# Kernel tuning notes

Measured on AMD Instinct MI355X. Metric: run time of the kernel, lower is better.

The kernel has to match this reference:

```python
import jax, jax.numpy as jnp
import numpy as np

B, S, H, E = 2, 4096, 2048, 8


def setup_inputs() -> dict:
    key = jax.random.key(0)
    k1, k2, k3 = jax.random.split(key, 3)
    x = jax.random.normal(k1, (B, S, H), dtype=jnp.float32)
    w_router = jax.random.normal(k2, (E, H), dtype=jnp.float32) * (1.0 / np.sqrt(H))
    # nn.Linear weight layout: [out_features, in_features] per expert -> [E, H, H]
    w_experts = jax.random.normal(k3, (E, H, H), dtype=jnp.float32) * (1.0 / np.sqrt(H))
    return {"x": x, "w_router": w_router, "w_experts": w_experts}


def reference(x, w_router, w_experts):
    # router logits: x @ W_r^T  -> [B, S, E]
    logits = jnp.einsum('bsh,eh->bse', x, w_router)
    idx = jnp.argmax(logits, axis=-1)  # [B, S] top-1 expert per token
    # dense all-expert outputs (matches original which evaluates every expert):
    # expert_e(x) = x @ W_e^T -> [B, S, E, H]
    all_out = jnp.einsum('bsh,efh->bsef', x, w_experts)
    # masked sum over one-hot mask == gather of the selected expert output
    out = jnp.take_along_axis(all_out, idx[:, :, None, None], axis=2)[:, :, 0, :]
    return out
```

## Files before the change

### kernel.cpp

```cpp
#include <hip/hip_runtime.h>
#include <hip/hip_bf16.h>
#include <cstdint>

#define T_TOK 8192
#define H_DIM 2048
#define N_EXP 8
#define FLAGBIT 0x80000000u

typedef __attribute__((ext_vector_type(4))) float f32x4;
typedef __attribute__((ext_vector_type(8))) short bf16x8;

__device__ __forceinline__ unsigned short f2bf(float f) {
  unsigned int u = __builtin_bit_cast(unsigned int, f);
  u += 0x7fffu + ((u >> 16) & 1u);
  return (unsigned short)(u >> 16);
}

#define GLL(SRC, DST) __builtin_amdgcn_global_load_lds( \
    (const __attribute__((address_space(1))) void*)(SRC), \
    (__attribute__((address_space(3))) void*)(DST), 16, 0, 0)

__global__ __launch_bounds__(256, 2) void k_conv(const float* __restrict__ we,
                                                 unsigned short* __restrict__ wb) {
  const size_t tix = ((size_t)blockIdx.x * 256 + threadIdx.x) * 8;
  const size_t stride = (size_t)2048 * 256 * 8;
  f32x4 v[16];
#pragma unroll
  for (int it = 0; it < 8; ++it) {
    v[2 * it]     = *reinterpret_cast<const f32x4*>(we + tix + (size_t)it * stride);
    v[2 * it + 1] = *reinterpret_cast<const f32x4*>(we + tix + (size_t)it * stride + 4);
  }
#pragma unroll
  for (int q = 0; q < 16; ++q) asm volatile("" : "+v"(v[q]));
#pragma unroll
  for (int it = 0; it < 8; ++it) {
    union { unsigned short h[8]; uint4 u; } r;
#pragma unroll
    for (int q = 0; q < 4; ++q) {
      r.h[q]     = f2bf(v[2 * it][q]);
      r.h[4 + q] = f2bf(v[2 * it + 1][q]);
    }
    *reinterpret_cast<uint4*>(wb + tix + (size_t)it * stride) = r.u;
  }
}

__global__ __launch_bounds__(256) void k_router(const float* __restrict__ x,
    const float* __restrict__ wr, unsigned short* __restrict__ xb,
    int* __restrict__ idx)
{
  __shared__ float swr[N_EXP * H_DIM];
#pragma unroll
  for (int i = 0; i < 16; ++i) {
    const int o = (threadIdx.x + i * 256) * 4;
    *reinterpret_cast<float4*>(&swr[o]) = *reinterpret_cast<const float4*>(&wr[o]);
  }
  __syncthreads();
  const int wv = threadIdx.x >> 6, lane = threadIdx.x & 63;
  const int t0 = (blockIdx.x * 4 + wv) * 4;
  float acc[4][N_EXP];
#pragma unroll
  for (int tt = 0; tt < 4; ++tt)
#pragma unroll
    for (int e = 0; e < N_EXP; ++e) acc[tt][e] = 0.f;
#pragma unroll
  for (int c = 0; c < H_DIM / 256; ++c) {
    const int h = c * 256 + lane * 4;
    float4 wvv[N_EXP];
#pragma unroll
    for (int e = 0; e < N_EXP; ++e)
      wvv[e] = *reinterpret_cast<const float4*>(&swr[e * H_DIM + h]);
#pragma unroll
    for (int tt = 0; tt < 4; ++tt) {
      const float4 xv = *reinterpret_cast<const float4*>(x + (size_t)(t0 + tt) * H_DIM + h);
      ushort4 bv;
      bv.x = f2bf(xv.x); bv.y = f2bf(xv.y); bv.z = f2bf(xv.z); bv.w = f2bf(xv.w);
      *reinterpret_cast<ushort4*>(xb + (size_t)(t0 + tt) * H_DIM + h) = bv;
#pragma unroll
      for (int e = 0; e < N_EXP; ++e) {
        acc[tt][e] = fmaf(xv.x, wvv[e].x, acc[tt][e]);
        acc[tt][e] = fmaf(xv.y, wvv[e].y, acc[tt][e]);
        acc[tt][e] = fmaf(xv.z, wvv[e].z, acc[tt][e]);
        acc[tt][e] = fmaf(xv.w, wvv[e].w, acc[tt][e]);
      }
    }
  }
#pragma unroll
  for (int off = 32; off >= 1; off >>= 1)
#pragma unroll
    for (int tt = 0; tt < 4; ++tt)
#pragma unroll
      for (int e = 0; e < N_EXP; ++e) acc[tt][e] += __shfl_xor(acc[tt][e], off, 64);
  if (lane == 0) {
#pragma unroll
    for (int tt = 0; tt < 4; ++tt) {
      float best = acc[tt][0]; int be = 0;
#pragma unroll
      for (int e = 1; e < N_EXP; ++e) if (acc[tt][e] > best) { best = acc[tt][e]; be = e; }
      idx[t0 + tt] = be;
    }
  }
}

__global__ __launch_bounds__(1024) void k_sort(const int* __restrict__ idx,
    int* __restrict__ tlist, int* __restrict__ estar, int* __restrict__ mlo,
    int* __restrict__ mhi, int* __restrict__ rpos, int* __restrict__ rtile,
    int* __restrict__ rtc)
{
  __shared__ int wc[N_EXP][128];
  __shared__ int wbase[N_EXP][128];
  __shared__ int sTot[N_EXP];
  __shared__ int off[N_EXP + 1];
  __shared__ int sE[32], sCnt[N_EXP], sBase[N_EXP];
  const int tid = threadIdx.x, w = tid >> 6, l = tid & 63;
  int myE[8];
#pragma unroll
  for (int j = 0; j < 8; ++j) {
    myE[j] = idx[j * 1024 + tid];
#pragma unroll
    for (int e = 0; e < N_EXP; ++e) {
      const unsigned long long bm = __ballot(myE[j] == e);
      if (l == e) wc[e][j * 16 + w] = __popcll(bm);
    }
  }
  __syncthreads();
  if (tid < N_EXP) {
    int s = 0;
    for (int k = 0; k < 128; ++k) { wbase[tid][k] = s; s += wc[tid][k]; }
    sTot[tid] = s;
  }
  __syncthreads();
  if (tid == 0) {
    off[0] = 0;
    for (int e = 0; e < N_EXP; ++e) off[e + 1] = off[e] + sTot[e];
  }
  __syncthreads();
#pragma unroll
  for (int j = 0; j < 8; ++j) {
    int rank = 0;
#pragma unroll
    for (int e = 0; e < N_EXP; ++e) {
      const unsigned long long bm = __ballot(myE[j] == e);
      if (myE[j] == e) rank = __popcll(bm & ((1ull << l) - 1ull));
    }
    tlist[off[myE[j]] + wbase[myE[j]][j * 16 + w] + rank] = j * 1024 + tid;
  }
  if (tid < 32) {
    const int lo = tid * 256, hi = lo + 256;
    int bl = -1, bE = 0, bLo = 0, bHi = 0;
#pragma unroll
    for (int e = 0; e < N_EXP; ++e) {
      const int a = off[e] > lo ? off[e] : lo;
      const int b = off[e + 1] < hi ? off[e + 1] : hi;
      if (b - a > bl) { bl = b - a; bE = e; bLo = a - lo; bHi = b - lo; }
    }
    sE[tid] = bE; estar[tid] = bE; mlo[tid] = bLo; mhi[tid] = bHi;
  }
  __syncthreads();
  if (tid < N_EXP) {
    int cnt = 0;
    for (int t = 0; t < 32; ++t) {
      if (sE[t] == tid) continue;
      const int lo = t * 256, hi = lo + 256;
      const int a = off[tid] > lo ? off[tid] : lo;
      const int b = off[tid + 1] < hi ? off[tid + 1] : hi;
      if (b > a) cnt += b - a;
    }
    sCnt[tid] = cnt;
  }
  __syncthreads();
  if (tid == 0) {
    int base = 0, ntile = 0;
    for (int e = 0; e < N_EXP; ++e) {
      sBase[e] = base;
      const int pt = (sCnt[e] + 127) >> 7;
      for (int k = 0; k < pt; ++k) rtile[ntile++] = e;
      base += pt << 7;
    }
    *rtc = ntile;
  }
  __syncthreads();
  if (tid < N_EXP && sCnt[tid] > 0) {
    int ptr = sBase[tid], firstp = -1;
    for (int t = 0; t < 32; ++t) {
      if (sE[t] == tid) continue;
      const int lo = t * 256, hi = lo + 256;
      const int a = off[tid] > lo ? off[tid] : lo;
      const int b = off[tid + 1] < hi ? off[tid + 1] : hi;
      for (int p = a; p < b; ++p) { if (firstp < 0) firstp = p; rpos[ptr++] = p; }
    }
    const int end = sBase[tid] + (((sCnt[tid] + 127) >> 7) << 7);
    for (; ptr < end; ++ptr) rpos[ptr] = (int)((unsigned)firstp | FLAGBIT);
  }
}

__global__ __launch_bounds__(256) void k_zero_min(const int* __restrict__ rpos,
    const int* __restrict__ tlist, const int* __restrict__ rtc,
    float* __restrict__ out)
{
  const int nslots = (*rtc) << 7;
  const float4 z = {0.f, 0.f, 0.f, 0.f};
  for (int s = blockIdx.x; s < nslots; s += 256) {
    const int ent = rpos[s];
    if ((unsigned)ent & FLAGBIT) continue;
    const int tok = tlist[ent];
    float* op = out + (size_t)tok * H_DIM;
    for (int i = threadIdx.x; i < H_DIM / 4; i += 256)
      reinterpret_cast<float4*>(op)[i] = z;
  }
}

template<int Q, bool LOADB, bool VMC>
__device__ __forceinline__ void gphase(const char* LP,
    __attribute__((address_space(3))) char* LDS3,
    int rdBase, int aRowOff, int bRowOff, int ch0, int ch1,
    bf16x8 (&bfr)[8], f32x4 (&acc)[8][4],
    const unsigned short* s0, const unsigned short* s1, int d0, int d1)
{
  if constexpr (LOADB) {
#pragma unroll
    for (int nf = 0; nf < 4; ++nf) {
      bfr[nf * 2 + 0] = *reinterpret_cast<const bf16x8*>(LP + rdBase + 32768 + bRowOff + nf * 2048 + ch0);
      bfr[nf * 2 + 1] = *reinterpret_cast<const bf16x8*>(LP + rdBase + 32768 + bRowOff + nf * 2048 + ch1);
    }
  }
  bf16x8 af[2][2];
#pragma unroll
  for (int m = 0; m < 2; ++m) {
    af[m][0] = *reinterpret_cast<const bf16x8*>(LP + rdBase + aRowOff + (2 * Q + m) * 2048 + ch0);
    af[m][1] = *reinterpret_cast<const bf16x8*>(LP + rdBase + aRowOff + (2 * Q + m) * 2048 + ch1);
  }
  GLL(s0, LDS3 + d0);
  GLL(s1, LDS3 + d1);
  __builtin_amdgcn_sched_barrier(0);
  __builtin_amdgcn_s_barrier();
  __builtin_amdgcn_sched_barrier(0);
  __builtin_amdgcn_s_setprio(1);
#pragma unroll
  for (int ks = 0; ks < 2; ++ks)
#pragma unroll
    for (int m = 0; m < 2; ++m)
#pragma unroll
      for (int nf = 0; nf < 4; ++nf)
        acc[2 * Q + m][nf] = __builtin_amdgcn_mfma_f32_16x16x32_bf16(af[m][ks], bfr[nf * 2 + ks], acc[2 * Q + m][nf], 0, 0, 0);
  __builtin_amdgcn_s_setprio(0);
  if constexpr (VMC) asm volatile("s_waitcnt vmcnt(4)" ::: "memory");
  __builtin_amdgcn_sched_barrier(0);
  __builtin_amdgcn_s_barrier();
  __builtin_amdgcn_sched_barrier(0);
}

__global__ __launch_bounds__(512, 2) void k_gemm(const unsigned short* __restrict__ xb,
    const unsigned short* __restrict__ wb, const int* __restrict__ tlist,
    const int* __restrict__ estar, const int* __restrict__ mlo, const int* __restrict__ mhi,
    const int* __restrict__ rpos, const int* __restrict__ rtile, const int* __restrict__ rtc,
    float* __restrict__ out)
{
  __shared__ short lds[65536];
  const int bid = blockIdx.x;
  const int tid = threadIdx.x;
  const int l = tid & 63, wv = tid >> 6;
  const int l16 = l & 15, g = l >> 4;
  const char* LP = (const char*)lds;
  auto* LDS3 = (__attribute__((address_space(3))) char*)lds;
  const int sw = l16 & 7;
  const int ch0 = ((0 + g) ^ sw) << 4;
  const int ch1 = ((4 + g) ^ sw) << 4;
  const int csrc = ((l & 7) ^ ((l >> 3) & 7)) * 8;
  const int srow = l >> 3;

  if (bid < 256) {
    const int mt = (bid & 7) * 4 + ((bid >> 3) & 3);
    const int nt = bid >> 5;
    const int m0 = mt * 256, f0 = nt * 256;
    const int e = estar[mt], mLo = mlo[mt], mHi = mhi[mt];
    const int wm = wv >> 2, wn = wv & 3;
    const int aRowOff = (wm * 128 + l16) * 128;
    const int bRowOff = (wn * 64 + l16) * 128;

    const unsigned short* aP[2][2];
    const unsigned short* bP[2][2];
    const unsigned short* wpan = wb + (size_t)e * H_DIM * H_DIM;
#pragma unroll
    for (int h = 0; h < 2; ++h)
#pragma unroll
      for (int j = 0; j < 2; ++j) {
        const int tok = tlist[m0 + h * 128 + (wv * 2 + j) * 8 + srow];
        aP[h][j] = xb + (size_t)tok * H_DIM + csrc;
        bP[h][j] = wpan + (size_t)(f0 + h * 128 + (wv * 2 + j) * 8 + srow) * H_DIM + csrc;
      }
    const int sl0 = wv * 2048, sl1 = wv * 2048 + 1024;

    f32x4 acc[8][4];
#pragma unroll
    for (int mf = 0; mf < 8; ++mf)
#pragma unroll
      for (int nf = 0; nf < 4; ++nf) acc[mf][nf] = (f32x4){0.f, 0.f, 0.f, 0.f};
    bf16x8 bfr[8];

    GLL(aP[0][0], LDS3 + 0 + sl0);      GLL(aP[0][1], LDS3 + 0 + sl1);
    GLL(aP[1][0], LDS3 + 16384 + sl0);  GLL(aP[1][1], LDS3 + 16384 + sl1);
    GLL(bP[0][0], LDS3 + 32768 + sl0);  GLL(bP[0][1], LDS3 + 32768 + sl1);
    GLL(bP[1][0], LDS3 + 49152 + sl0);  GLL(bP[1][1], LDS3 + 49152 + sl1);
    GLL(bP[0][0] + 64, LDS3 + 65536 + 32768 + sl0);  GLL(bP[0][1] + 64, LDS3 + 65536 + 32768 + sl1);
    GLL(bP[1][0] + 64, LDS3 + 65536 + 49152 + sl0);  GLL(bP[1][1] + 64, LDS3 + 65536 + 49152 + sl1);
    asm volatile("s_waitcnt vmcnt(4)" ::: "memory");
    __builtin_amdgcn_sched_barrier(0);
    __builtin_amdgcn_s_barrier();
    __builtin_amdgcn_sched_barrier(0);

    for (int i = 0; i < 16; ++i) {
      const int kk1 = ((2 * i + 1) << 6) & (H_DIM - 1);
      const int kk2 = ((2 * i + 2) << 6) & (H_DIM - 1);
      const int kk3 = ((2 * i + 3) << 6) & (H_DIM - 1);
      gphase<0, true , false>(LP, LDS3, 0, aRowOff, bRowOff, ch0, ch1, bfr, acc,
          aP[0][0] + kk1, aP[0][1] + kk1, 65536 + 0 + sl0, 65536 + 0 + sl1);
      gphase<1, false, false>(LP, LDS3, 0, aRowOff, bRowOff, ch0, ch1, bfr, acc,
          aP[1][0] + kk1, aP[1][1] + kk1, 65536 + 16384 + sl0, 65536 + 16384 + sl1);
      gphase<2, false, false>(LP, LDS3, 0, aRowOff, bRowOff, ch0, ch1, bfr, acc,
          bP[0][0] + kk2, bP[0][1] + kk2, 0 + 32768 + sl0, 0 + 32768 + sl1);
      gphase<3, false, true >(LP, LDS3, 0, aRowOff, bRowOff, ch0, ch1, bfr, acc,
          bP[1][0] + kk2, bP[1][1] + kk2, 0 + 49152 + sl0, 0 + 49152 + sl1);
      gphase<0, true , false>(LP, LDS3, 65536, aRowOff, bRowOff, ch0, ch1, bfr, acc,
          aP[0][0] + kk2, aP[0][1] + kk2, 0 + 0 + sl0, 0 + 0 + sl1);
      gphase<1, false, false>(LP, LDS3, 65536, aRowOff, bRowOff, ch0, ch1, bfr, acc,
          aP[1][0] + kk2, aP[1][1] + kk2, 0 + 16384 + sl0, 0 + 16384 + sl1);
      gphase<2, false, false>(LP, LDS3, 65536, aRowOff, bRowOff, ch0, ch1, bfr, acc,
          bP[0][0] + kk3, bP[0][1] + kk3, 65536 + 32768 + sl0, 65536 + 32768 + sl1);
      gphase<3, false, true >(LP, LDS3, 65536, aRowOff, bRowOff, ch0, ch1, bfr, acc,
          bP[1][0] + kk3, bP[1][1] + kk3, 65536 + 49152 + sl0, 65536 + 49152 + sl1);
    }

#pragma unroll
    for (int mf = 0; mf < 8; ++mf) {
#pragma unroll
      for (int r = 0; r < 4; ++r) {
        const int row = wm * 128 + mf * 16 + g * 4 + r;
        if (row >= mLo && row < mHi) {
          const int t = tlist[m0 + row];
          float* op = out + (size_t)t * H_DIM + f0 + wn * 64 + l16;
#pragma unroll
          for (int nf = 0; nf < 4; ++nf) op[nf * 16] = acc[mf][nf][r];
        }
      }
    }
    return;
  }

  const int bid2 = bid - 256;
  const int bx = bid2 >> 4;
  if (bx >= *rtc) return;
  const int f0 = ((bid2 >> 1) & 7) * 256;
  const int kc = bid2 & 1;
  const int e = rtile[bx];
  const int wm = wv >> 2, wn = wv & 3;

  const unsigned short* aS[2];
#pragma unroll
  for (int j = 0; j < 2; ++j) {
    const int ent = rpos[bx * 128 + (wv * 2 + j) * 8 + srow];
    const int tok = tlist[ent & 0x7fffffff];
    aS[j] = xb + (size_t)tok * H_DIM + csrc;
  }
  const unsigned short* bS[4];
#pragma unroll
  for (int j = 0; j < 4; ++j)
    bS[j] = wb + (size_t)e * H_DIM * H_DIM + (size_t)(f0 + (wv * 4 + j) * 8 + srow) * H_DIM + csrc;

  f32x4 acc[4][4];
#pragma unroll
  for (int mf = 0; mf < 4; ++mf)
#pragma unroll
    for (int nf = 0; nf < 4; ++nf) acc[mf][nf] = (f32x4){0.f, 0.f, 0.f, 0.f};

  for (int it = 0; it < 16; ++it) {
    const int kk = kc * 1024 + it * 64;
    __syncthreads();
#pragma unroll
    for (int j = 0; j < 2; ++j) GLL(aS[j] + kk, LDS3 + (wv * 2 + j) * 1024);
#pragma unroll
    for (int j = 0; j < 4; ++j) GLL(bS[j] + kk, LDS3 + 16384 + (wv * 4 + j) * 1024);
    __syncthreads();
    bf16x8 af[4][2];
#pragma unroll
    for (int mf = 0; mf < 4; ++mf) {
      af[mf][0] = *reinterpret_cast<const bf16x8*>(LP + (wm * 64 + mf * 16 + l16) * 128 + ch0);
      af[mf][1] = *reinterpret_cast<const bf16x8*>(LP + (wm * 64 + mf * 16 + l16) * 128 + ch1);
    }
#pragma unroll
    for (int nf = 0; nf < 4; ++nf) {
      const bf16x8 b0 = *reinterpret_cast<const bf16x8*>(LP + 16384 + (wn * 64 + nf * 16 + l16) * 128 + ch0);
      const bf16x8 b1 = *reinterpret_cast<const bf16x8*>(LP + 16384 + (wn * 64 + nf * 16 + l16) * 128 + ch1);
#pragma unroll
      for (int mf = 0; mf < 4; ++mf) {
        acc[mf][nf] = __builtin_amdgcn_mfma_f32_16x16x32_bf16(af[mf][0], b0, acc[mf][nf], 0, 0, 0);
        acc[mf][nf] = __builtin_amdgcn_mfma_f32_16x16x32_bf16(af[mf][1], b1, acc[mf][nf], 0, 0, 0);
      }
    }
  }
#pragma unroll
  for (int mf = 0; mf < 4; ++mf) {
#pragma unroll
    for (int r = 0; r < 4; ++r) {
      const int row = wm * 64 + mf * 16 + g * 4 + r;
      const int ent = rpos[bx * 128 + row];
      if (!((unsigned)ent & FLAGBIT)) {
        const int tok = tlist[ent];
        float* op = out + (size_t)tok * H_DIM + f0 + wn * 64 + l16;
#pragma unroll
        for (int nf = 0; nf < 4; ++nf) atomicAdd(op + nf * 16, acc[mf][nf][r]);
      }
    }
  }
}

extern "C" void kernel_launch(void* const* d_in, const int* in_sizes, int n_in,
                              void* d_out, int out_size, void* d_ws, size_t ws_size,
                              hipStream_t stream) {
  const float* x  = (const float*)d_in[0];
  const float* wr = (const float*)d_in[1];
  const float* we = (const float*)d_in[2];
  float* out = (float*)d_out;

  char* p = (char*)d_ws;
  unsigned short* xb = (unsigned short*)p; p += (size_t)T_TOK * H_DIM * 2;
  unsigned short* wb = (unsigned short*)p; p += (size_t)N_EXP * H_DIM * H_DIM * 2;
  int* idx    = (int*)p; p += T_TOK * 4;
  int* tlist  = (int*)p; p += T_TOK * 4;
  int* rpos   = (int*)p; p += T_TOK * 4;
  int* estar  = (int*)p; p += 32 * 4;
  int* mlo    = (int*)p; p += 32 * 4;
  int* mhi    = (int*)p; p += 32 * 4;
  int* rtile  = (int*)p; p += 64 * 4;
  int* rtc    = (int*)p; p += 64;

  k_conv<<<2048, 256, 0, stream>>>(we, wb);
  k_router<<<512, 256, 0, stream>>>(x, wr, xb, idx);
  k_sort<<<1, 1024, 0, stream>>>(idx, tlist, estar, mlo, mhi, rpos, rtile, rtc);
  k_zero_min<<<256, 256, 0, stream>>>(rpos, tlist, rtc, out);
  k_gemm<<<256 + 1024, 512, 0, stream>>>(xb, wb, tlist, estar, mlo, mhi, rpos, rtile, rtc, out);
}
```

Baseline: 194.1 us.

## Retile expert GEMM to 16 waves with 4-stage K-ring buffer

```diff
diff --git a/kernel.cpp b/kernel.cpp
--- a/kernel.cpp
+++ b/kernel.cpp
@@ -209,47 +209,7 @@
   }
 }
 
-template<int Q, bool LOADB, bool VMC>
-__device__ __forceinline__ void gphase(const char* LP,
-    __attribute__((address_space(3))) char* LDS3,
-    int rdBase, int aRowOff, int bRowOff, int ch0, int ch1,
-    bf16x8 (&bfr)[8], f32x4 (&acc)[8][4],
-    const unsigned short* s0, const unsigned short* s1, int d0, int d1)
-{
-  if constexpr (LOADB) {
-#pragma unroll
-    for (int nf = 0; nf < 4; ++nf) {
-      bfr[nf * 2 + 0] = *reinterpret_cast<const bf16x8*>(LP + rdBase + 32768 + bRowOff + nf * 2048 + ch0);
-      bfr[nf * 2 + 1] = *reinterpret_cast<const bf16x8*>(LP + rdBase + 32768 + bRowOff + nf * 2048 + ch1);
-    }
-  }
-  bf16x8 af[2][2];
-#pragma unroll
-  for (int m = 0; m < 2; ++m) {
-    af[m][0] = *reinterpret_cast<const bf16x8*>(LP + rdBase + aRowOff + (2 * Q + m) * 2048 + ch0);
-    af[m][1] = *reinterpret_cast<const bf16x8*>(LP + rdBase + aRowOff + (2 * Q + m) * 2048 + ch1);
-  }
-  GLL(s0, LDS3 + d0);
-  GLL(s1, LDS3 + d1);
-  __builtin_amdgcn_sched_barrier(0);
-  __builtin_amdgcn_s_barrier();
-  __builtin_amdgcn_sched_barrier(0);
-  __builtin_amdgcn_s_setprio(1);
-#pragma unroll
-  for (int ks = 0; ks < 2; ++ks)
-#pragma unroll
-    for (int m = 0; m < 2; ++m)
-#pragma unroll
-      for (int nf = 0; nf < 4; ++nf)
-        acc[2 * Q + m][nf] = __builtin_amdgcn_mfma_f32_16x16x32_bf16(af[m][ks], bfr[nf * 2 + ks], acc[2 * Q + m][nf], 0, 0, 0);
-  __builtin_amdgcn_s_setprio(0);
-  if constexpr (VMC) asm volatile("s_waitcnt vmcnt(4)" ::: "memory");
-  __builtin_amdgcn_sched_barrier(0);
-  __builtin_amdgcn_s_barrier();
-  __builtin_amdgcn_sched_barrier(0);
-}
-
-__global__ __launch_bounds__(512, 2) void k_gemm(const unsigned short* __restrict__ xb,
+__global__ __launch_bounds__(1024, 4) void k_gemm(const unsigned short* __restrict__ xb,
     const unsigned short* __restrict__ wb, const int* __restrict__ tlist,
     const int* __restrict__ estar, const int* __restrict__ mlo, const int* __restrict__ mhi,
     const int* __restrict__ rpos, const int* __restrict__ rtile, const int* __restrict__ rtc,
@@ -259,14 +219,9 @@
   const int bid = blockIdx.x;
   const int tid = threadIdx.x;
   const int l = tid & 63, wv = tid >> 6;
-  const int l16 = l & 15, g = l >> 4;
+  const int l16 = l & 15, g16 = l >> 4;
   const char* LP = (const char*)lds;
   auto* LDS3 = (__attribute__((address_space(3))) char*)lds;
-  const int sw = l16 & 7;
-  const int ch0 = ((0 + g) ^ sw) << 4;
-  const int ch1 = ((4 + g) ^ sw) << 4;
-  const int csrc = ((l & 7) ^ ((l >> 3) & 7)) * 8;
-  const int srow = l >> 3;
 
   if (bid < 256) {
     const int mt = (bid & 7) * 4 + ((bid >> 3) & 3);
@@ -274,70 +229,71 @@
     const int m0 = mt * 256, f0 = nt * 256;
     const int e = estar[mt], mLo = mlo[mt], mHi = mhi[mt];
     const int wm = wv >> 2, wn = wv & 3;
-    const int aRowOff = (wm * 128 + l16) * 128;
-    const int bRowOff = (wn * 64 + l16) * 128;
-
-    const unsigned short* aP[2][2];
-    const unsigned short* bP[2][2];
-    const unsigned short* wpan = wb + (size_t)e * H_DIM * H_DIM;
-#pragma unroll
-    for (int h = 0; h < 2; ++h)
-#pragma unroll
-      for (int j = 0; j < 2; ++j) {
-        const int tok = tlist[m0 + h * 128 + (wv * 2 + j) * 8 + srow];
-        aP[h][j] = xb + (size_t)tok * H_DIM + csrc;
-        bP[h][j] = wpan + (size_t)(f0 + h * 128 + (wv * 2 + j) * 8 + srow) * H_DIM + csrc;
-      }
-    const int sl0 = wv * 2048, sl1 = wv * 2048 + 1024;
-
-    f32x4 acc[8][4];
-#pragma unroll
-    for (int mf = 0; mf < 8; ++mf)
+
+    const int ch = (g16 ^ ((l16 >> 1) & 3)) << 4;
+    const int aRd = (wm * 64 + l16) * 64 + ch;
+    const int bRd = 16384 + (wn * 64 + l16) * 64 + ch;
+
+    const int csrc = (((l & 3) ^ ((l >> 3) & 3))) * 8;
+    const int srow = l >> 2;
+    const int tokA = tlist[m0 + wv * 16 + srow];
+    const unsigned short* aS = xb + (size_t)tokA * H_DIM + csrc;
+    const unsigned short* bS = wb + (size_t)e * H_DIM * H_DIM
+                                  + (size_t)(f0 + wv * 16 + srow) * H_DIM + csrc;
+    const int dA = wv * 1024;
+    const int dB = 16384 + wv * 1024;
+
+    f32x4 acc[4][4];
+#pragma unroll
+    for (int mf = 0; mf < 4; ++mf)
 #pragma unroll
       for (int nf = 0; nf < 4; ++nf) acc[mf][nf] = (f32x4){0.f, 0.f, 0.f, 0.f};
-    bf16x8 bfr[8];
-
-    GLL(aP[0][0], LDS3 + 0 + sl0);      GLL(aP[0][1], LDS3 + 0 + sl1);
-    GLL(aP[1][0], LDS3 + 16384 + sl0);  GLL(aP[1][1], LDS3 + 16384 + sl1);
-    GLL(bP[0][0], LDS3 + 32768 + sl0);  GLL(bP[0][1], LDS3 + 32768 + sl1);
-    GLL(bP[1][0], LDS3 + 49152 + sl0);  GLL(bP[1][1], LDS3 + 49152 + sl1);
-    GLL(bP[0][0] + 64, LDS3 + 65536 + 32768 + sl0);  GLL(bP[0][1] + 64, LDS3 + 65536 + 32768 + sl1);
-    GLL(bP[1][0] + 64, LDS3 + 65536 + 49152 + sl0);  GLL(bP[1][1] + 64, LDS3 + 65536 + 49152 + sl1);
+
+    GLL(aS +  0, LDS3 + 0 * 32768 + dA);  GLL(bS +  0, LDS3 + 0 * 32768 + dB);
+    GLL(aS + 32, LDS3 + 1 * 32768 + dA);  GLL(bS + 32, LDS3 + 1 * 32768 + dB);
+    GLL(aS + 64, LDS3 + 2 * 32768 + dA);  GLL(bS + 64, LDS3 + 2 * 32768 + dB);
     asm volatile("s_waitcnt vmcnt(4)" ::: "memory");
     __builtin_amdgcn_sched_barrier(0);
     __builtin_amdgcn_s_barrier();
     __builtin_amdgcn_sched_barrier(0);
 
-    for (int i = 0; i < 16; ++i) {
-      const int kk1 = ((2 * i + 1) << 6) & (H_DIM - 1);
-      const int kk2 = ((2 * i + 2) << 6) & (H_DIM - 1);
-      const int kk3 = ((2 * i + 3) << 6) & (H_DIM - 1);
-      gphase<0, true , false>(LP, LDS3, 0, aRowOff, bRowOff, ch0, ch1, bfr, acc,
-          aP[0][0] + kk1, aP[0][1] + kk1, 65536 + 0 + sl0, 65536 + 0 + sl1);
-      gphase<1, false, false>(LP, LDS3, 0, aRowOff, bRowOff, ch0, ch1, bfr, acc,
-          aP[1][0] + kk1, aP[1][1] + kk1, 65536 + 16384 + sl0, 65536 + 16384 + sl1);
-      gphase<2, false, false>(LP, LDS3, 0, aRowOff, bRowOff, ch0, ch1, bfr, acc,
-          bP[0][0] + kk2, bP[0][1] + kk2, 0 + 32768 + sl0, 0 + 32768 + sl1);
-      gphase<3, false, true >(LP, LDS3, 0, aRowOff, bRowOff, ch0, ch1, bfr, acc,
-          bP[1][0] + kk2, bP[1][1] + kk2, 0 + 49152 + sl0, 0 + 49152 + sl1);
-      gphase<0, true , false>(LP, LDS3, 65536, aRowOff, bRowOff, ch0, ch1, bfr, acc,
-          aP[0][0] + kk2, aP[0][1] + kk2, 0 + 0 + sl0, 0 + 0 + sl1);
-      gphase<1, false, false>(LP, LDS3, 65536, aRowOff, bRowOff, ch0, ch1, bfr, acc,
-          aP[1][0] + kk2, aP[1][1] + kk2, 0 + 16384 + sl0, 0 + 16384 + sl1);
-      gphase<2, false, false>(LP, LDS3, 65536, aRowOff, bRowOff, ch0, ch1, bfr, acc,
-          bP[0][0] + kk3, bP[0][1] + kk3, 65536 + 32768 + sl0, 65536 + 32768 + sl1);
-      gphase<3, false, true >(LP, LDS3, 65536, aRowOff, bRowOff, ch0, ch1, bfr, acc,
-          bP[1][0] + kk3, bP[1][1] + kk3, 65536 + 49152 + sl0, 65536 + 49152 + sl1);
-    }
-
-#pragma unroll
-    for (int mf = 0; mf < 8; ++mf) {
+    for (int t = 0; t < 64; ++t) {
+      const int buf  = (t & 3) * 32768;
+      const int nbuf = ((t + 3) & 3) * 32768;
+      const int kk   = ((t + 3) & 63) * 32;
+      bf16x8 af[4], bf[4];
+#pragma unroll
+      for (int mf = 0; mf < 4; ++mf)
+        af[mf] = *reinterpret_cast<const bf16x8*>(LP + buf + aRd + mf * 1024);
+#pragma unroll
+      for (int nf = 0; nf < 4; ++nf)
+        bf[nf] = *reinterpret_cast<const bf16x8*>(LP + buf + bRd + nf * 1024);
+      GLL(aS + kk, LDS3 + nbuf + dA);
+      GLL(bS + kk, LDS3 + nbuf + dB);
+      __builtin_amdgcn_sched_barrier(0);
+      __builtin_amdgcn_s_barrier();
+      __builtin_amdgcn_sched_barrier(0);
+      __builtin_amdgcn_s_setprio(1);
+#pragma unroll
+      for (int mf = 0; mf < 4; ++mf)
+#pragma unroll
+        for (int nf = 0; nf < 4; ++nf)
+          acc[mf][nf] = __builtin_amdgcn_mfma_f32_16x16x32_bf16(af[mf], bf[nf], acc[mf][nf], 0, 0, 0);
+      __builtin_amdgcn_s_setprio(0);
+      asm volatile("s_waitcnt vmcnt(4)" ::: "memory");
+      __builtin_amdgcn_sched_barrier(0);
+      __builtin_amdgcn_s_barrier();
+      __builtin_amdgcn_sched_barrier(0);
+    }
+
+#pragma unroll
+    for (int mf = 0; mf < 4; ++mf) {
 #pragma unroll
       for (int r = 0; r < 4; ++r) {
-        const int row = wm * 128 + mf * 16 + g * 4 + r;
+        const int row = wm * 64 + mf * 16 + g16 * 4 + r;
         if (row >= mLo && row < mHi) {
-          const int t = tlist[m0 + row];
-          float* op = out + (size_t)t * H_DIM + f0 + wn * 64 + l16;
+          const int t2 = tlist[m0 + row];
+          float* op = out + (size_t)t2 * H_DIM + f0 + wn * 64 + l16;
 #pragma unroll
           for (int nf = 0; nf < 4; ++nf) op[nf * 16] = acc[mf][nf][r];
         }
@@ -353,55 +309,56 @@
   const int kc = bid2 & 1;
   const int e = rtile[bx];
   const int wm = wv >> 2, wn = wv & 3;
-
-  const unsigned short* aS[2];
-#pragma unroll
-  for (int j = 0; j < 2; ++j) {
-    const int ent = rpos[bx * 128 + (wv * 2 + j) * 8 + srow];
+  const int sw = l16 & 7;
+  const int ch0 = ((0 + g16) ^ sw) << 4, ch1 = ((4 + g16) ^ sw) << 4;
+  const int csrc8 = ((l & 7) ^ ((l >> 3) & 7)) * 8;
+  const int srow8 = l >> 3;
+
+  const unsigned short* aS;
+  {
+    const int ent = rpos[bx * 128 + wv * 8 + srow8];
     const int tok = tlist[ent & 0x7fffffff];
-    aS[j] = xb + (size_t)tok * H_DIM + csrc;
-  }
-  const unsigned short* bS[4];
-#pragma unroll
-  for (int j = 0; j < 4; ++j)
-    bS[j] = wb + (size_t)e * H_DIM * H_DIM + (size_t)(f0 + (wv * 4 + j) * 8 + srow) * H_DIM + csrc;
-
-  f32x4 acc[4][4];
-#pragma unroll
-  for (int mf = 0; mf < 4; ++mf)
+    aS = xb + (size_t)tok * H_DIM + csrc8;
+  }
+  const unsigned short* bS0 = wb + (size_t)e * H_DIM * H_DIM
+                                 + (size_t)(f0 + wv * 8 + srow8) * H_DIM + csrc8;
+  const unsigned short* bS1 = bS0 + (size_t)128 * H_DIM;
+
+  f32x4 acc[2][4];
+#pragma unroll
+  for (int mf = 0; mf < 2; ++mf)
 #pragma unroll
     for (int nf = 0; nf < 4; ++nf) acc[mf][nf] = (f32x4){0.f, 0.f, 0.f, 0.f};
 
   for (int it = 0; it < 16; ++it) {
     const int kk = kc * 1024 + it * 64;
     __syncthreads();
-#pragma unroll
-    for (int j = 0; j < 2; ++j) GLL(aS[j] + kk, LDS3 + (wv * 2 + j) * 1024);
-#pragma unroll
-    for (int j = 0; j < 4; ++j) GLL(bS[j] + kk, LDS3 + 16384 + (wv * 4 + j) * 1024);
+    GLL(aS + kk, LDS3 + wv * 1024);
+    GLL(bS0 + kk, LDS3 + 16384 + wv * 1024);
+    GLL(bS1 + kk, LDS3 + 16384 + 16384 + wv * 1024);
     __syncthreads();
-    bf16x8 af[4][2];
-#pragma unroll
-    for (int mf = 0; mf < 4; ++mf) {
-      af[mf][0] = *reinterpret_cast<const bf16x8*>(LP + (wm * 64 + mf * 16 + l16) * 128 + ch0);
-      af[mf][1] = *reinterpret_cast<const bf16x8*>(LP + (wm * 64 + mf * 16 + l16) * 128 + ch1);
+    bf16x8 af[2][2];
+#pragma unroll
+    for (int mf = 0; mf < 2; ++mf) {
+      af[mf][0] = *reinterpret_cast<const bf16x8*>(LP + (wm * 32 + mf * 16 + l16) * 128 + ch0);
+      af[mf][1] = *reinterpret_cast<const bf16x8*>(LP + (wm * 32 + mf * 16 + l16) * 128 + ch1);
     }
 #pragma unroll
     for (int nf = 0; nf < 4; ++nf) {
       const bf16x8 b0 = *reinterpret_cast<const bf16x8*>(LP + 16384 + (wn * 64 + nf * 16 + l16) * 128 + ch0);
       const bf16x8 b1 = *reinterpret_cast<const bf16x8*>(LP + 16384 + (wn * 64 + nf * 16 + l16) * 128 + ch1);
 #pragma unroll
-      for (int mf = 0; mf < 4; ++mf) {
+      for (int mf = 0; mf < 2; ++mf) {
         acc[mf][nf] = __builtin_amdgcn_mfma_f32_16x16x32_bf16(af[mf][0], b0, acc[mf][nf], 0, 0, 0);
         acc[mf][nf] = __builtin_amdgcn_mfma_f32_16x16x32_bf16(af[mf][1], b1, acc[mf][nf], 0, 0, 0);
       }
     }
   }
 #pragma unroll
-  for (int mf = 0; mf < 4; ++mf) {
+  for (int mf = 0; mf < 2; ++mf) {
 #pragma unroll
     for (int r = 0; r < 4; ++r) {
-      const int row = wm * 64 + mf * 16 + g * 4 + r;
+      const int row = wm * 32 + mf * 16 + g16 * 4 + r;
       const int ent = rpos[bx * 128 + row];
       if (!((unsigned)ent & FLAGBIT)) {
         const int tok = tlist[ent];
@@ -437,5 +394,5 @@
   k_router<<<512, 256, 0, stream>>>(x, wr, xb, idx);
   k_sort<<<1, 1024, 0, stream>>>(idx, tlist, estar, mlo, mhi, rpos, rtile, rtc);
   k_zero_min<<<256, 256, 0, stream>>>(rpos, tlist, rtc, out);
-  k_gemm<<<256 + 1024, 512, 0, stream>>>(xb, wb, tlist, estar, mlo, mhi, rpos, rtile, rtc, out);
-}
+  k_gemm<<<256 + 1024, 1024, 0, stream>>>(xb, wb, tlist, estar, mlo, mhi, rpos, rtile, rtc, out);
+}
```

New measurement: 194.2 us. Within noise of the previous version (+0.1%).
